# Optimization experiments

Hardware: AMD Instinct MI355X
Metric: run time of the kernel (lower is better)

Reference implementation:

```python
import jax, jax.numpy as jnp
import numpy as np

HEADS = 16
DIM_HEAD = 64
SCALE = DIM_HEAD ** -0.5
MASK_NEG = 1000000.0


def setup_inputs() -> dict:
    key = jax.random.key(0)
    ks = jax.random.split(key, 6)
    B, N, M, D = 2, 2048, 2048, 1024
    inner = HEADS * DIM_HEAD  # 1024
    x = jax.random.normal(ks[0], (B, N, D), dtype=jnp.float32)
    context = jax.random.normal(ks[1], (B, M, D), dtype=jnp.float32)
    mask = jax.random.randint(ks[2], (B, N), 0, 2, dtype=jnp.int32)
    Wq = jax.random.normal(ks[3], (D, inner), dtype=jnp.float32) * (D ** -0.5)
    Wkv = jax.random.normal(ks[4], (D, 2 * inner), dtype=jnp.float32) * (D ** -0.5)
    Wout = jax.random.normal(ks[5], (inner, D), dtype=jnp.float32) * (inner ** -0.5)
    bout = jnp.zeros((D,), dtype=jnp.float32)
    return {"x": x, "context": context, "mask": mask,
            "Wq": Wq, "Wkv": Wkv, "Wout": Wout, "bout": bout}


def _split_heads(t):
    # [b, n, (h d)] -> [b, h, n, d]
    b, n, _ = t.shape
    return t.reshape(b, n, HEADS, DIM_HEAD).transpose(0, 2, 1, 3)


def reference(x, context, mask, Wq, Wkv, Wout, bout):
    kv = context @ Wkv                      # [b, m, 2*inner]
    k, v = jnp.split(kv, 2, axis=-1)
    q = x @ Wq                              # [b, n, inner]
    q, k, v = _split_heads(q), _split_heads(k), _split_heads(v)
    dots = jnp.einsum('bhnd,bhmd->bhnm', q, k) * SCALE
    # mask is [b, n]: additive penalty per query row (faithful to source)
    dots = dots - (1.0 - mask.astype(jnp.float32))[:, None, :, None] * MASK_NEG
    attn = jax.nn.softmax(dots, axis=-1)
    out = jnp.einsum('bhnm,bhmd->bhnd', attn, v)  # [b, h, n, d]
    b, h, n, d = out.shape
    out = out.transpose(0, 2, 1, 3).reshape(b, n, h * d)
    return out @ Wout + bout
```

## Files before the change

### kernel.cpp

```cpp
#include <hip/hip_runtime.h>
#include <hip/hip_bf16.h>
#include <math.h>

#define BATCH   2
#define NQ      2048
#define NKV     2048
#define DMODEL  1024
#define HEADS   16
#define INNER   1024
#define KVCOLS  2048

typedef short bf16x8 __attribute__((ext_vector_type(8)));
typedef float f32x4  __attribute__((ext_vector_type(4)));

__device__ __forceinline__ short f2bf(float x) {
    __hip_bfloat16 h = __float2bfloat16(x);
    return *reinterpret_cast<short*>(&h);
}
__device__ __forceinline__ float bf2f(short h) {
    unsigned int u = ((unsigned int)(unsigned short)h) << 16;
    float f;
    __builtin_memcpy(&f, &u, 4);
    return f;
}
__device__ __forceinline__ void gl_lds16(const void* g, void* l) {
    __builtin_amdgcn_global_load_lds(
        (const __attribute__((address_space(1))) unsigned int*)g,
        (__attribute__((address_space(3))) unsigned int*)l, 16, 0, 0);
}
__device__ __forceinline__ int sw(int row, int chunk) {
    return row * 64 + ((chunk ^ (row & 7)) << 3);
}

__device__ __forceinline__ void split_chunk(const float* __restrict__ in,
                                            short* __restrict__ hi,
                                            short* __restrict__ lo, int id)
{
    const int i = (id * 256 + (int)threadIdx.x) * 4;
    float4 v = *(const float4*)(in + i);
    short4 h, l;
    h.x = f2bf(v.x); l.x = f2bf(v.x - bf2f(h.x));
    h.y = f2bf(v.y); l.y = f2bf(v.y - bf2f(h.y));
    h.z = f2bf(v.z); l.z = f2bf(v.z - bf2f(h.z));
    h.w = f2bf(v.w); l.w = f2bf(v.w - bf2f(h.w));
    *(short4*)(hi + i) = h;
    *(short4*)(lo + i) = l;
}

__device__ __forceinline__ void tile_transpose_split(
    const float* __restrict__ W, short* __restrict__ Wth, short* __restrict__ Wtl,
    int Kd, int Nd, int bx, int by, int split)
{
    __shared__ float t[32][33];
    const int lx = threadIdx.x & 31, ly = threadIdx.x >> 5;
    #pragma unroll
    for (int j = 0; j < 4; ++j)
        t[ly + j * 8][lx] = W[(size_t)(by * 32 + ly + j * 8) * Nd + bx * 32 + lx];
    __syncthreads();
    #pragma unroll
    for (int j = 0; j < 4; ++j) {
        const float v = t[lx][ly + j * 8];
        const short h = f2bf(v);
        const size_t idx = (size_t)(bx * 32 + ly + j * 8) * Kd + by * 32 + lx;
        Wth[idx] = h;
        if (split) Wtl[idx] = f2bf(v - bf2f(h));
    }
}

__global__ __launch_bounds__(256)
void prep_all(const float* __restrict__ x, const float* __restrict__ ctx,
              const float* __restrict__ Wq, const float* __restrict__ Wkv,
              const float* __restrict__ Wout,
              short* __restrict__ xh, short* __restrict__ xl,
              short* __restrict__ ch, short* __restrict__ cl,
              short* __restrict__ WqTh, short* __restrict__ WqTl,
              short* __restrict__ WkvTh, short* __restrict__ WkvTl,
              short* __restrict__ WoutT)
{
    const int id = blockIdx.x;
    if (id < 4096) {
        split_chunk(x, xh, xl, id);
    } else if (id < 8192) {
        split_chunk(ctx, ch, cl, id - 4096);
    } else {
        const int r = id - 8192;
        if (r < 1024)
            tile_transpose_split(Wq, WqTh, WqTl, 1024, 1024, r & 31, r >> 5, 1);
        else if (r < 3072)
            tile_transpose_split(Wkv, WkvTh, WkvTl, 1024, 2048, (r - 1024) & 63, (r - 1024) >> 6, 1);
        else
            tile_transpose_split(Wout, WoutT, nullptr, 1024, 1024, (r - 3072) & 31, (r - 3072) >> 5, 0);
    }
}

__global__ __launch_bounds__(256)
void qkv_gemm(const short* __restrict__ xh, const short* __restrict__ xl,
              const short* __restrict__ ch, const short* __restrict__ cl,
              const short* __restrict__ WqTh, const short* __restrict__ WqTl,
              const short* __restrict__ WkvTh, const short* __restrict__ WkvTl,
              short* __restrict__ qhp, short* __restrict__ qlp,
              short* __restrict__ khp, short* __restrict__ klp,
              short* __restrict__ vp)
{
    __shared__ short Ash[128 * 32];
    __shared__ short Asl[128 * 32];
    __shared__ short Bsh[128 * 32];
    __shared__ short Bsl[128 * 32];

    const int tid = threadIdx.x;
    const int z = blockIdx.z;
    const int m0 = blockIdx.y * 128, n0 = blockIdx.x * 128;
    const int w = tid >> 6, ln = tid & 63;
    const int wm = (w & 1) * 64, wn = (w >> 1) * 64;
    const int lr = ln & 15, lq = ln >> 4;
    const int terms = (z == 2) ? 1 : 3;

    const short* Ah  = (z == 0) ? xh : ch;
    const short* Al  = (z == 0) ? xl : cl;
    const short* Bth = (z == 0) ? WqTh : (z == 1 ? WkvTh : WkvTh + (size_t)1024 * 1024);
    const short* Btl = (z == 0) ? WqTl : WkvTl;

    f32x4 acc[4][4];
    #pragma unroll
    for (int mt = 0; mt < 4; ++mt)
        #pragma unroll
        for (int nt = 0; nt < 4; ++nt)
            #pragma unroll
            for (int r = 0; r < 4; ++r) acc[mt][nt][r] = 0.0f;

    for (int k0 = 0; k0 < 1024; k0 += 32) {
        __syncthreads();
        #pragma unroll
        for (int it = 0; it < 2; ++it) {
            const int f = it * 256 + tid;
            const int row = f >> 2, c = f & 3;
            const int cg = c ^ ((row >> 1) & 3);
            const size_t ao = (size_t)(m0 + row) * 1024 + k0 + cg * 8;
            const size_t bo = (size_t)(n0 + row) * 1024 + k0 + cg * 8;
            gl_lds16(Ah  + ao, Ash + f * 8);
            gl_lds16(Bth + bo, Bsh + f * 8);
            if (terms == 3) {
                gl_lds16(Al  + ao, Asl + f * 8);
                gl_lds16(Btl + bo, Bsl + f * 8);
            }
        }
        __syncthreads();

        bf16x8 ah[4], bh[4];
        #pragma unroll
        for (int t = 0; t < 4; ++t) {
            const int ar = wm + t * 16 + lr;
            const int br = wn + t * 16 + lr;
            ah[t] = *(const bf16x8*)(Ash + ar * 32 + ((lq ^ ((ar >> 1) & 3)) << 3));
            bh[t] = *(const bf16x8*)(Bsh + br * 32 + ((lq ^ ((br >> 1) & 3)) << 3));
        }
        #pragma unroll
        for (int mt = 0; mt < 4; ++mt)
            #pragma unroll
            for (int nt = 0; nt < 4; ++nt)
                acc[mt][nt] = __builtin_amdgcn_mfma_f32_16x16x32_bf16(
                    ah[mt], bh[nt], acc[mt][nt], 0, 0, 0);

        if (terms == 3) {
            bf16x8 al[4], bl[4];
            #pragma unroll
            for (int t = 0; t < 4; ++t) {
                const int ar = wm + t * 16 + lr;
                const int br = wn + t * 16 + lr;
                al[t] = *(const bf16x8*)(Asl + ar * 32 + ((lq ^ ((ar >> 1) & 3)) << 3));
                bl[t] = *(const bf16x8*)(Bsl + br * 32 + ((lq ^ ((br >> 1) & 3)) << 3));
            }
            #pragma unroll
            for (int mt = 0; mt < 4; ++mt)
                #pragma unroll
                for (int nt = 0; nt < 4; ++nt) {
                    acc[mt][nt] = __builtin_amdgcn_mfma_f32_16x16x32_bf16(
                        ah[mt], bl[nt], acc[mt][nt], 0, 0, 0);
                    acc[mt][nt] = __builtin_amdgcn_mfma_f32_16x16x32_bf16(
                        al[mt], bh[nt], acc[mt][nt], 0, 0, 0);
                }
        }
    }

    const float scale = (z == 0) ? 2.0f : 1.0f;
    short* Chi = (z == 0) ? qhp : (z == 1 ? khp : vp);
    short* Clo = (z == 0) ? qlp : klp;
    #pragma unroll
    for (int mt = 0; mt < 4; ++mt)
        #pragma unroll
        for (int nt = 0; nt < 4; ++nt)
            #pragma unroll
            for (int r = 0; r < 4; ++r) {
                const int row = m0 + wm + mt * 16 + lq * 4 + r;
                const int col = n0 + wn + nt * 16 + lr;
                const float v = acc[mt][nt][r] * scale;
                const short hh = f2bf(v);
                Chi[(size_t)row * 1024 + col] = hh;
                if (z != 2)
                    Clo[(size_t)row * 1024 + col] = f2bf(v - bf2f(hh));
            }
}

__global__ __launch_bounds__(256)
void gemm_out(const short* __restrict__ A, const short* __restrict__ Bt,
              float* __restrict__ C, const float* __restrict__ bias)
{
    __shared__ short As[128 * 64];
    __shared__ short Bs[64 * 64];
    const int tid = threadIdx.x;
    const int m0 = blockIdx.y * 128, n0 = blockIdx.x * 64;
    const int w = tid >> 6, ln = tid & 63;
    const int wm = (w & 1) * 64, wn = (w >> 1) * 32;
    const int lr = ln & 15, lq = ln >> 4;

    f32x4 acc[4][2];
    #pragma unroll
    for (int mt = 0; mt < 4; ++mt)
        #pragma unroll
        for (int nt = 0; nt < 2; ++nt)
            #pragma unroll
            for (int r = 0; r < 4; ++r) acc[mt][nt][r] = 0.0f;

    for (int k0 = 0; k0 < 1024; k0 += 64) {
        __syncthreads();
        #pragma unroll
        for (int it = 0; it < 4; ++it) {
            const int f = it * 256 + tid;
            const int row = f >> 3, c8 = f & 7;
            const int cg = c8 ^ (row & 7);
            gl_lds16(A + (size_t)(m0 + row) * 1024 + k0 + cg * 8, As + f * 8);
        }
        #pragma unroll
        for (int it = 0; it < 2; ++it) {
            const int f = it * 256 + tid;
            const int row = f >> 3, c8 = f & 7;
            const int cg = c8 ^ (row & 7);
            gl_lds16(Bt + (size_t)(n0 + row) * 1024 + k0 + cg * 8, Bs + f * 8);
        }
        __syncthreads();
        #pragma unroll
        for (int ks = 0; ks < 2; ++ks) {
            bf16x8 af[4], bfr[2];
            #pragma unroll
            for (int t = 0; t < 4; ++t) {
                const int ar = wm + t * 16 + lr;
                af[t] = *(const bf16x8*)(As + ar * 64 + (((ks * 4 + lq) ^ (ar & 7)) << 3));
            }
            #pragma unroll
            for (int t = 0; t < 2; ++t) {
                const int br = wn + t * 16 + lr;
                bfr[t] = *(const bf16x8*)(Bs + br * 64 + (((ks * 4 + lq) ^ (br & 7)) << 3));
            }
            #pragma unroll
            for (int mt = 0; mt < 4; ++mt)
                #pragma unroll
                for (int nt = 0; nt < 2; ++nt)
                    acc[mt][nt] = __builtin_amdgcn_mfma_f32_16x16x32_bf16(
                        af[mt], bfr[nt], acc[mt][nt], 0, 0, 0);
        }
    }
    #pragma unroll
    for (int mt = 0; mt < 4; ++mt)
        #pragma unroll
        for (int nt = 0; nt < 2; ++nt)
            #pragma unroll
            for (int r = 0; r < 4; ++r) {
                const int row = m0 + wm + mt * 16 + lq * 4 + r;
                const int col = n0 + wn + nt * 16 + lr;
                C[(size_t)row * 1024 + col] = acc[mt][nt][r] + bias[col];
            }
}

__device__ __forceinline__ void vwrite(int* __restrict__ vt32, int dg4, int slot,
                                       int2 a, int2 b)
{
    const short* as = (const short*)&a;
    const short* bs = (const short*)&b;
    #pragma unroll
    for (int j = 0; j < 4; ++j)
        vt32[(dg4 + j) * 32 + (((slot >> 2) ^ ((dg4 + j) & 7)) << 2) + (slot & 3)] =
            (int)((unsigned short)as[j] | ((unsigned int)(unsigned short)bs[j] << 16));
}

__global__ __launch_bounds__(512, 4)
void flash_v10(const short* __restrict__ qh, const short* __restrict__ ql,
               const short* __restrict__ kh, const short* __restrict__ kl,
               const short* __restrict__ vp, const int* __restrict__ mask,
               short* __restrict__ aob)
{
    const int qt = blockIdx.x, h = blockIdx.y, b = blockIdx.z;
    const int tid = threadIdx.x;
    const int w = tid >> 6, ln = tid & 63;
    const int lr = ln & 15, lq = ln >> 4;

    __shared__ short Kh[2 * 4096];
    __shared__ short Kl[2 * 4096];
    __shared__ short Vt[2 * 4096];

    const size_t qrow0 = (size_t)(b * NQ + qt * 128);

    bf16x8 aqh[2], aql[2];
    #pragma unroll
    for (int ks = 0; ks < 2; ++ks) {
        const size_t qoff = (qrow0 + w * 16 + lr) * INNER + h * 64 + ks * 32 + lq * 8;
        aqh[ks] = *(const bf16x8*)(qh + qoff);
        aql[ks] = *(const bf16x8*)(ql + qoff);
    }
    const float bmag = mask[b * NQ + qt * 128 + w * 16 + lr] ? 0.0f : 12582912.0f;

    bf16x8 vone;
    #pragma unroll
    for (int j = 0; j < 8; ++j) vone[j] = (short)0x3F80;

    const int krow = tid >> 3, kc = tid & 7;
    const int kcg = kc ^ (krow & 7);
    const size_t koff0 = ((size_t)(b * NKV + krow)) * INNER + h * 64 + kcg * 8;

    const int idx = tid & 31, dg4 = (tid >> 5) * 4;
    const int tp = idx & 15;
    const int vkey = ((tp >> 2) << 2) + 2 * (tp & 1) + (((tp >> 1) & 1) << 4)
                   + ((idx >> 4) << 5);
    int2 rva, rvb;

    {
        const short* v0 = vp + (size_t)(b * NKV + vkey) * INNER + h * 64 + dg4;
        rva = *(const int2*)(v0);
        rvb = *(const int2*)(v0 + INNER);
        gl_lds16(kh + koff0, Kh + tid * 8);
        gl_lds16(kl + koff0, Kl + tid * 8);
        vwrite((int*)Vt, dg4, idx, rva, rvb);
    }

    f32x4 oacc[4];
    #pragma unroll
    for (int dg = 0; dg < 4; ++dg)
        #pragma unroll
        for (int r = 0; r < 4; ++r) oacc[dg][r] = 0.0f;
    f32x4 pacc;
    #pragma unroll
    for (int r = 0; r < 4; ++r) pacc[r] = 0.0f;

    const float C16 = 1.44269504f * 0.0625f;

    for (int kt = 0; kt < NKV / 64; ++kt) {
        const int cur = kt & 1;
        __syncthreads();

        if (kt < NKV / 64 - 1) {
            const size_t kadd = (size_t)((kt + 1) * 64) * INNER;
            const short* v0 = vp + (size_t)(b * NKV + (kt + 1) * 64 + vkey) * INNER + h * 64 + dg4;
            rva = *(const int2*)(v0);
            rvb = *(const int2*)(v0 + INNER);
            const int nb = (cur ^ 1) * 4096;
            gl_lds16(kh + koff0 + kadd, Kh + nb + tid * 8);
            gl_lds16(kl + koff0 + kadd, Kl + nb + tid * 8);
        }

        const short* KhC = Kh + cur * 4096;
        const short* KlC = Kl + cur * 4096;
        const short* VtC = Vt + cur * 4096;

        f32x4 sacc[4];
        #pragma unroll
        for (int g = 0; g < 4; ++g)
            #pragma unroll
            for (int r = 0; r < 4; ++r) sacc[g][r] = 0.0f;
        __builtin_amdgcn_s_setprio(1);
        #pragma unroll
        for (int ks = 0; ks < 2; ++ks) {
            #pragma unroll
            for (int g = 0; g < 4; ++g) {
                const bf16x8 bkh = *(const bf16x8*)(KhC + sw(g * 16 + lr, ks * 4 + lq));
                const bf16x8 bkl = *(const bf16x8*)(KlC + sw(g * 16 + lr, ks * 4 + lq));
                sacc[g] = __builtin_amdgcn_mfma_f32_16x16x32_bf16(bkh, aqh[ks], sacc[g], 0, 0, 0);
                sacc[g] = __builtin_amdgcn_mfma_f32_16x16x32_bf16(bkl, aqh[ks], sacc[g], 0, 0, 0);
                sacc[g] = __builtin_amdgcn_mfma_f32_16x16x32_bf16(bkh, aql[ks], sacc[g], 0, 0, 0);
            }
        }
        __builtin_amdgcn_s_setprio(0);

        bf16x8 ap[2];
        #pragma unroll
        for (int ks = 0; ks < 2; ++ks) {
            bf16x8 a;
            #pragma unroll
            for (int g2 = 0; g2 < 2; ++g2)
                #pragma unroll
                for (int r = 0; r < 4; ++r) {
                    const float sq = (sacc[2 * ks + g2][r] + bmag) - bmag;
                    const float xx = sq * C16;
                    float pv;
                    asm("v_exp_f32 %0, %1" : "=v"(pv) : "v"(xx));
                    a[g2 * 4 + r] = f2bf(pv);
                }
            ap[ks] = a;
        }

        __builtin_amdgcn_s_setprio(1);
        #pragma unroll
        for (int ks = 0; ks < 2; ++ks) {
            pacc = __builtin_amdgcn_mfma_f32_16x16x32_bf16(ap[ks], vone, pacc, 0, 0, 0);
            #pragma unroll
            for (int dg = 0; dg < 4; ++dg) {
                const bf16x8 bv = *(const bf16x8*)(VtC + sw(dg * 16 + lr, ks * 4 + lq));
                oacc[dg] = __builtin_amdgcn_mfma_f32_16x16x32_bf16(ap[ks], bv, oacc[dg], 0, 0, 0);
            }
        }
        __builtin_amdgcn_s_setprio(0);

        if (kt < NKV / 64 - 1) {
            vwrite((int*)(Vt + (cur ^ 1) * 4096), dg4, idx, rva, rvb);
        }
    }

    float pinv[4];
    #pragma unroll
    for (int r = 0; r < 4; ++r) pinv[r] = 1.0f / pacc[r];

    #pragma unroll
    for (int dg = 0; dg < 4; ++dg)
        #pragma unroll
        for (int r = 0; r < 4; ++r) {
            const int row = w * 16 + lq * 4 + r;
            aob[(qrow0 + row) * INNER + h * 64 + dg * 16 + lr] =
                f2bf(oacc[dg][r] * pinv[r]);
        }
}

extern "C" void kernel_launch(void* const* d_in, const int* in_sizes, int n_in,
                              void* d_out, int out_size, void* d_ws, size_t ws_size,
                              hipStream_t stream)
{
    const float* x    = (const float*)d_in[0];
    const float* ctx  = (const float*)d_in[1];
    const int*   mask = (const int*)d_in[2];
    const float* Wq   = (const float*)d_in[3];
    const float* Wkv  = (const float*)d_in[4];
    const float* Wout = (const float*)d_in[5];
    const float* bout = (const float*)d_in[6];
    float* out = (float*)d_out;

    short* base  = (short*)d_ws;
    short* xh    = base;
    short* xl    = base + (size_t)4 * 1024 * 1024;
    short* aob   = xh;
    short* WqTh  = base + (size_t) 8 * 1024 * 1024;
    short* WqTl  = base + (size_t) 9 * 1024 * 1024;
    short* qhp   = base + (size_t)10 * 1024 * 1024;
    short* qlp   = base + (size_t)14 * 1024 * 1024;
    short* WkvTh = base + (size_t)18 * 1024 * 1024;
    short* WkvTl = base + (size_t)20 * 1024 * 1024;
    short* khp   = base + (size_t)22 * 1024 * 1024;
    short* klp   = base + (size_t)26 * 1024 * 1024;
    short* WoutT = base + (size_t)30 * 1024 * 1024;
    short* ch    = base + (size_t)31 * 1024 * 1024;
    short* cl    = base + (size_t)35 * 1024 * 1024;
    short* vp    = base + (size_t)39 * 1024 * 1024;

    const dim3 blk(256);
    prep_all<<<12288, blk, 0, stream>>>(x, ctx, Wq, Wkv, Wout,
                                        xh, xl, ch, cl,
                                        WqTh, WqTl, WkvTh, WkvTl, WoutT);
    qkv_gemm<<<dim3(8, 32, 3), blk, 0, stream>>>(
        xh, xl, ch, cl, WqTh, WqTl, WkvTh, WkvTl,
        qhp, qlp, khp, klp, vp);
    flash_v10<<<dim3(NQ / 128, HEADS, BATCH), dim3(512), 0, stream>>>(
        qhp, qlp, khp, klp, vp, mask, aob);
    gemm_out<<<dim3(1024 / 64, 4096 / 128), blk, 0, stream>>>(
        aob, WoutT, out, bout);
}
```

Before: 252.2 us.

## Software-pipeline PV matmul one tile behind QK with triple-buffered V

Restructures the flash attention loop so the P·V MFMAs for the previous key tile are issued right after the current tile's QK^T MFMAs, before the exp/convert of the current scores. V shared memory goes from double to triple buffering so the lagged tile's V stays valid while the next one is written, and an epilogue handles the last tile. The aim is to overlap the exp/VALU work with MFMA work across iterations. In exchange it uses more LDS and keeps the previous P fragments live in registers, which could lower occupancy.

```diff
diff --git a/kernel.cpp b/kernel.cpp
--- a/kernel.cpp
+++ b/kernel.cpp
@@ -283,7 +283,7 @@
 }
 
 __global__ __launch_bounds__(512, 4)
-void flash_v10(const short* __restrict__ qh, const short* __restrict__ ql,
+void flash_v11(const short* __restrict__ qh, const short* __restrict__ ql,
                const short* __restrict__ kh, const short* __restrict__ kl,
                const short* __restrict__ vp, const int* __restrict__ mask,
                short* __restrict__ aob)
@@ -295,7 +295,7 @@
 
     __shared__ short Kh[2 * 4096];
     __shared__ short Kl[2 * 4096];
-    __shared__ short Vt[2 * 4096];
+    __shared__ short Vt[3 * 4096];
 
     const size_t qrow0 = (size_t)(b * NQ + qt * 128);
 
@@ -341,6 +341,10 @@
     for (int r = 0; r < 4; ++r) pacc[r] = 0.0f;
 
     const float C16 = 1.44269504f * 0.0625f;
+
+    bf16x8 apA[2];
+    int vpv = 2;
+    int vwr = 1;
 
     for (int kt = 0; kt < NKV / 64; ++kt) {
         const int cur = kt & 1;
@@ -358,7 +362,6 @@
 
         const short* KhC = Kh + cur * 4096;
         const short* KlC = Kl + cur * 4096;
-        const short* VtC = Vt + cur * 4096;
 
         f32x4 sacc[4];
         #pragma unroll
@@ -379,7 +382,21 @@
         }
         __builtin_amdgcn_s_setprio(0);
 
-        bf16x8 ap[2];
+        if (kt > 0) {
+            const short* VtP = Vt + vpv * 4096;
+            __builtin_amdgcn_s_setprio(1);
+            #pragma unroll
+            for (int ks = 0; ks < 2; ++ks) {
+                pacc = __builtin_amdgcn_mfma_f32_16x16x32_bf16(apA[ks], vone, pacc, 0, 0, 0);
+                #pragma unroll
+                for (int dg = 0; dg < 4; ++dg) {
+                    const bf16x8 bv = *(const bf16x8*)(VtP + sw(dg * 16 + lr, ks * 4 + lq));
+                    oacc[dg] = __builtin_amdgcn_mfma_f32_16x16x32_bf16(apA[ks], bv, oacc[dg], 0, 0, 0);
+                }
+            }
+            __builtin_amdgcn_s_setprio(0);
+        }
+
         #pragma unroll
         for (int ks = 0; ks < 2; ++ks) {
             bf16x8 a;
@@ -393,23 +410,27 @@
                     asm("v_exp_f32 %0, %1" : "=v"(pv) : "v"(xx));
                     a[g2 * 4 + r] = f2bf(pv);
                 }
-            ap[ks] = a;
-        }
-
-        __builtin_amdgcn_s_setprio(1);
+            apA[ks] = a;
+        }
+
+        if (kt < NKV / 64 - 1) {
+            vwrite((int*)(Vt + vwr * 4096), dg4, idx, rva, rvb);
+        }
+
+        vpv = (vpv == 2) ? 0 : vpv + 1;
+        vwr = (vwr == 2) ? 0 : vwr + 1;
+    }
+
+    {
+        const short* VtP = Vt + vpv * 4096;
         #pragma unroll
         for (int ks = 0; ks < 2; ++ks) {
-            pacc = __builtin_amdgcn_mfma_f32_16x16x32_bf16(ap[ks], vone, pacc, 0, 0, 0);
+            pacc = __builtin_amdgcn_mfma_f32_16x16x32_bf16(apA[ks], vone, pacc, 0, 0, 0);
             #pragma unroll
             for (int dg = 0; dg < 4; ++dg) {
-                const bf16x8 bv = *(const bf16x8*)(VtC + sw(dg * 16 + lr, ks * 4 + lq));
-                oacc[dg] = __builtin_amdgcn_mfma_f32_16x16x32_bf16(ap[ks], bv, oacc[dg], 0, 0, 0);
-            }
-        }
-        __builtin_amdgcn_s_setprio(0);
-
-        if (kt < NKV / 64 - 1) {
-            vwrite((int*)(Vt + (cur ^ 1) * 4096), dg4, idx, rva, rvb);
+                const bf16x8 bv = *(const bf16x8*)(VtP + sw(dg * 16 + lr, ks * 4 + lq));
+                oacc[dg] = __builtin_amdgcn_mfma_f32_16x16x32_bf16(apA[ks], bv, oacc[dg], 0, 0, 0);
+            }
         }
     }
 
@@ -464,7 +485,7 @@
     qkv_gemm<<<dim3(8, 32, 3), blk, 0, stream>>>(
         xh, xl, ch, cl, WqTh, WqTl, WkvTh, WkvTl,
         qhp, qlp, khp, klp, vp);
-    flash_v10<<<dim3(NQ / 128, HEADS, BATCH), dim3(512), 0, stream>>>(
+    flash_v11<<<dim3(NQ / 128, HEADS, BATCH), dim3(512), 0, stream>>>(
         qhp, qlp, khp, klp, vp, mask, aob);
     gemm_out<<<dim3(1024 / 64, 4096 / 128), blk, 0, stream>>>(
         aob, WoutT, out, bout);
```

After: 258.3 us. 2.4% more time.
